# Kernel optimization log

Hardware: AMD Instinct MI355X
Metric: run time of the kernel (lower is better)

## Reference

```python
import jax, jax.numpy as jnp
import numpy as np

# From init_kwargs betti_numbers = [[1,0],[1,1],[2,0],[1,2]]
GOOD_INTERVALS_0 = jnp.array([1, 1, 2, 1], dtype=jnp.int32)  # betti_0 per class
GOOD_INTERVALS_1 = jnp.array([0, 1, 0, 2], dtype=jnp.int32)  # betti_1 per class


def setup_inputs() -> dict:
    key = jax.random.key(0)
    k1, k2, k3 = jax.random.split(key, 3)
    B, C, H, W, N = 16, 4, 512, 512, 8192
    prediction = jax.random.normal(k1, (B, C, H, W), dtype=jnp.float32)
    intervals_comp_0 = jax.random.randint(k2, (B, C, N, 2, 2), 0, H, dtype=jnp.int32)
    intervals_comp_1 = jax.random.randint(k3, (B, C, N, 2, 2), 0, H, dtype=jnp.int32)
    return {
        "prediction": prediction,
        "intervals_comp_0": intervals_comp_0,
        "intervals_comp_1": intervals_comp_1,
    }


def _compute_interval_diff(prediction, intervals, num_comps):
    # prediction: (B, C, H, W); intervals: (B, C, N, 2, 2) int; num_comps: (C,) int
    B, C, N = intervals.shape[:3]
    b_idx = jnp.arange(B)[:, None, None]  # (B,1,1)
    c_idx = jnp.arange(C)[None, :, None]  # (1,C,1)
    birth = prediction[b_idx, c_idx, intervals[..., 0, 0], intervals[..., 0, 1]]  # (B,C,N)
    death = prediction[b_idx, c_idx, intervals[..., 1, 0], intervals[..., 1, 1]]  # (B,C,N)
    diff = (birth - death) ** 2
    # first min(num_comps[c], N) intervals per (b,c) are "good": loss is 1 - diff there
    good = jnp.arange(N)[None, None, :] < jnp.minimum(num_comps, N)[None, :, None]  # (1,C,N)
    diff = jnp.where(good, 1.0 - diff, diff)
    return jnp.sum(diff)


def reference(prediction, intervals_comp_0, intervals_comp_1):
    loss_0 = _compute_interval_diff(prediction, intervals_comp_0, GOOD_INTERVALS_0)
    loss_1 = _compute_interval_diff(prediction, intervals_comp_1, GOOD_INTERVALS_1)
    return loss_0 + loss_1
```

## Files before the change

### kernel.cpp

```cpp
#include <hip/hip_runtime.h>

constexpr int Bn = 16, Cn = 4, Hn = 512, Wn = 512, Nn = 8192;
constexpr int BLOCK = 256;
constexpr int GRID  = 1024;
constexpr int PHASES = 4;

__device__ __forceinline__ int good_of(int s, int c) {
    return (s == 0) ? ((c == 2) ? 2 : 1)
                    : ((c == 1) ? 1 : ((c == 3) ? 2 : 0));
}

__global__ __launch_bounds__(BLOCK) void bd_gather(
        const float* __restrict__ pred,
        const int4* __restrict__ iv0,
        const int4* __restrict__ iv1,
        float* __restrict__ partials) {
    const int m   = blockIdx.x;
    const int xcd = m & 7;
    const int r   = m >> 3;
    const int idx = r * BLOCK + threadIdx.x;
    const int u   = idx >> 14;
    const int s   = (idx >> 13) & 1;
    const int e   = idx & (Nn - 1);

    const int4* __restrict__ iv = s ? iv1 : iv0;

    float acc = 0.0f;
    #pragma unroll 1
    for (int j = 0; j < PHASES; ++j) {
        const int p = (2 * j + u) * 8 + xcd;
        const int c = p & (Cn - 1);
        const float* __restrict__ plane = pred + (size_t)p * (Hn * Wn);

        int4 a = iv[p * Nn + e];
        float birth = plane[(a.x << 9) + a.y];
        float death = plane[(a.z << 9) + a.w];
        float d = birth - death; d *= d;
        acc += (e < good_of(s, c)) ? (1.0f - d) : d;

        __syncthreads();
    }

    #pragma unroll
    for (int off = 32; off > 0; off >>= 1)
        acc += __shfl_down(acc, off, 64);

    __shared__ float wsum[BLOCK / 64];
    const int lane = threadIdx.x & 63;
    const int wave = threadIdx.x >> 6;
    if (lane == 0) wsum[wave] = acc;
    __syncthreads();
    if (threadIdx.x == 0)
        partials[blockIdx.x] = wsum[0] + wsum[1] + wsum[2] + wsum[3];
}

__global__ __launch_bounds__(BLOCK) void bd_final(
        const float* __restrict__ partials,
        float* __restrict__ out) {
    float acc = 0.0f;
    #pragma unroll
    for (int i = 0; i < GRID / BLOCK; ++i)
        acc += partials[threadIdx.x + i * BLOCK];

    #pragma unroll
    for (int off = 32; off > 0; off >>= 1)
        acc += __shfl_down(acc, off, 64);

    __shared__ float wsum[BLOCK / 64];
    const int lane = threadIdx.x & 63;
    const int wave = threadIdx.x >> 6;
    if (lane == 0) wsum[wave] = acc;
    __syncthreads();
    if (threadIdx.x == 0)
        out[0] = wsum[0] + wsum[1] + wsum[2] + wsum[3];
}

extern "C" void kernel_launch(void* const* d_in, const int* in_sizes, int n_in,
                              void* d_out, int out_size, void* d_ws, size_t ws_size,
                              hipStream_t stream) {
    const float* pred = (const float*)d_in[0];
    const int4*  iv0  = (const int4*)d_in[1];
    const int4*  iv1  = (const int4*)d_in[2];
    float* out      = (float*)d_out;
    float* partials = (float*)d_ws;

    bd_gather<<<GRID, BLOCK, 0, stream>>>(pred, iv0, iv1, partials);
    bd_final<<<1, BLOCK, 0, stream>>>(partials, out);
}
```

Before: 109.4 us.

## Batch all phase loads up front and drop per-phase barriers

Loads the interval records for all four phases with nontemporal loads first, then issues all eight prediction gathers, and only then does the arithmetic. It also removes the per-phase __syncthreads, so loads from different phases can be in flight at once instead of one dependent load chain per phase. Keeping all phases live costs more registers. The nontemporal hint keeps the streamed interval data from evicting cache lines that the prediction gathers might reuse.

```diff
diff --git a/kernel.cpp b/kernel.cpp
--- a/kernel.cpp
+++ b/kernel.cpp
@@ -4,6 +4,8 @@
 constexpr int BLOCK = 256;
 constexpr int GRID  = 1024;
 constexpr int PHASES = 4;
+
+typedef int iv4 __attribute__((ext_vector_type(4)));
 
 __device__ __forceinline__ int good_of(int s, int c) {
     return (s == 0) ? ((c == 2) ? 2 : 1)
@@ -12,8 +14,8 @@
 
 __global__ __launch_bounds__(BLOCK) void bd_gather(
         const float* __restrict__ pred,
-        const int4* __restrict__ iv0,
-        const int4* __restrict__ iv1,
+        const iv4* __restrict__ iv0,
+        const iv4* __restrict__ iv1,
         float* __restrict__ partials) {
     const int m   = blockIdx.x;
     const int xcd = m & 7;
@@ -23,22 +25,31 @@
     const int s   = (idx >> 13) & 1;
     const int e   = idx & (Nn - 1);
 
-    const int4* __restrict__ iv = s ? iv1 : iv0;
+    const iv4* __restrict__ iv = s ? iv1 : iv0;
+
+    iv4 A[PHASES];
+    #pragma unroll
+    for (int j = 0; j < PHASES; ++j) {
+        const int p = (2 * j + u) * 8 + xcd;
+        A[j] = __builtin_nontemporal_load(&iv[p * Nn + e]);
+    }
+
+    float bs[PHASES], ds[PHASES];
+    #pragma unroll
+    for (int j = 0; j < PHASES; ++j) {
+        const int p = (2 * j + u) * 8 + xcd;
+        const float* __restrict__ plane = pred + (size_t)p * (Hn * Wn);
+        bs[j] = plane[(A[j].x << 9) + A[j].y];
+        ds[j] = plane[(A[j].z << 9) + A[j].w];
+    }
 
     float acc = 0.0f;
-    #pragma unroll 1
+    #pragma unroll
     for (int j = 0; j < PHASES; ++j) {
         const int p = (2 * j + u) * 8 + xcd;
         const int c = p & (Cn - 1);
-        const float* __restrict__ plane = pred + (size_t)p * (Hn * Wn);
-
-        int4 a = iv[p * Nn + e];
-        float birth = plane[(a.x << 9) + a.y];
-        float death = plane[(a.z << 9) + a.w];
-        float d = birth - death; d *= d;
+        float d = bs[j] - ds[j]; d *= d;
         acc += (e < good_of(s, c)) ? (1.0f - d) : d;
-
-        __syncthreads();
     }
 
     #pragma unroll
@@ -79,8 +90,8 @@
                               void* d_out, int out_size, void* d_ws, size_t ws_size,
                               hipStream_t stream) {
     const float* pred = (const float*)d_in[0];
-    const int4*  iv0  = (const int4*)d_in[1];
-    const int4*  iv1  = (const int4*)d_in[2];
+    const iv4*   iv0  = (const iv4*)d_in[1];
+    const iv4*   iv1  = (const iv4*)d_in[2];
     float* out      = (float*)d_out;
     float* partials = (float*)d_ws;
 
```

Result: slower. 112.0 us (+2.4%).
